# Kernel optimization log

Hardware: AMD Instinct MI355X
Metric: run time of the kernel (lower is better)

The kernel has to match this reference:

```python
import jax, jax.numpy as jnp
import numpy as np

B = 65536
N_HOSTS = 16
N_FEATS = 48        # 3 * n_hosts
N_WINDOW = 3
N_LATENT = 10
GAT_IN = 3
GAT_OUT = 16
E = N_WINDOW + GAT_OUT  # 19, MHA embed dim
PROTO_DIM = 10


def setup_inputs() -> dict:
    key = jax.random.key(0)
    ks = jax.random.split(key, 20)
    def rn(k, shape, scale=0.1):
        return jax.random.normal(k, shape, dtype=jnp.float32) * scale
    return {
        "t": jax.random.normal(ks[0], (B, N_WINDOW, N_FEATS), dtype=jnp.float32),
        "s": jnp.zeros((1,), jnp.float32),  # unused by forward, kept for signature fidelity
        "h0": jax.random.normal(ks[1], (B, 1, N_WINDOW), dtype=jnp.float32),
        "gru_Wih": rn(ks[2], (3 * N_WINDOW, N_FEATS)),
        "gru_Whh": rn(ks[3], (3 * N_WINDOW, N_WINDOW)),
        "gru_bih": rn(ks[4], (3 * N_WINDOW,)),
        "gru_bhh": rn(ks[5], (3 * N_WINDOW,)),
        "gat_W": rn(ks[6], (GAT_IN, GAT_OUT)),
        "gat_al": rn(ks[7], (GAT_OUT,)),
        "gat_ar": rn(ks[8], (GAT_OUT,)),
        "mha_Win": rn(ks[9], (3 * E, E)),
        "mha_bin": rn(ks[10], (3 * E,)),
        "mha_Wout": rn(ks[11], (E, E)),
        "mha_bout": rn(ks[12], (E,)),
        "enc_W": rn(ks[13], (N_HOSTS * N_LATENT, N_WINDOW * E)),
        "enc_b": rn(ks[14], (N_HOSTS * N_LATENT,)),
        "anom_W": rn(ks[15], (2, N_LATENT)),
        "anom_b": rn(ks[16], (2,)),
        "proto_W": rn(ks[17], (PROTO_DIM, N_LATENT)),
        "proto_b": rn(ks[18], (PROTO_DIM,)),
    }


def _forward(t, s, h0, gru_Wih, gru_Whh, gru_bih, gru_bhh,
             gat_W, gat_al, gat_ar, mha_Win, mha_bin, mha_Wout, mha_bout,
             enc_W, enc_b, anom_W, anom_b, proto_W, proto_b):
    # ---- GRU (seq-first, batch B, hidden = n_window = 3) ----
    xs = jnp.swapaxes(t, 0, 1)  # (3, B, 48)
    h0_ = h0[:, 0, :]           # (B, 3)

    def gru_step(h, x_t):
        gi = x_t @ gru_Wih.T + gru_bih   # (B, 9)
        gh = h @ gru_Whh.T + gru_bhh     # (B, 9)
        i_r, i_z, i_n = jnp.split(gi, 3, axis=-1)
        h_r, h_z, h_n = jnp.split(gh, 3, axis=-1)
        r = jax.nn.sigmoid(i_r + h_r)
        z = jax.nn.sigmoid(i_z + h_z)
        n = jnp.tanh(i_n + r * h_n)
        h_new = (1.0 - z) * n + z * h
        return h_new, h_new

    _, gru_out = jax.lax.scan(gru_step, h0_, xs)  # (3, B, 3)

    # ---- GAT on fully-connected 16-node graph (with self loops) ----
    gin = t.reshape(t.shape[0], N_WINDOW, N_HOSTS, GAT_IN)      # (B, 3, 16, 3)
    z = jnp.einsum("bwnc,cf->bwnf", gin, gat_W)                 # (B, 3, 16, 16)
    el = z @ gat_al                                              # src scores (B,3,16)
    er = z @ gat_ar                                              # dst scores (B,3,16)
    e = jax.nn.leaky_relu(er[..., :, None] + el[..., None, :], 0.2)  # (B,3,v,u)
    alpha = jax.nn.softmax(e, axis=-1)                           # softmax over sources u
    gat_nodes = jnp.einsum("bwvu,bwuf->bwvf", alpha, z)          # (B, 3, 16, 16)
    gat_out = gat_nodes.mean(axis=2)                             # (B, 3, 16) mean over hosts
    gat_out = jnp.swapaxes(gat_out, 0, 1)                        # (3, B, 16)

    # ---- concat + single-head MHA (embed=19) ----
    c = jnp.concatenate([gru_out, gat_out], axis=-1)             # (3, B, 19)
    Wq, Wk, Wv = jnp.split(mha_Win, 3, axis=0)
    bq, bk, bv = jnp.split(mha_bin, 3, axis=0)
    q = c @ Wq.T + bq
    k = c @ Wk.T + bk
    v = c @ Wv.T + bv
    scores = jnp.einsum("sbe,tbe->bst", q, k) / jnp.sqrt(jnp.float32(E))
    attw = jax.nn.softmax(scores, axis=-1)
    attn = jnp.einsum("bst,tbe->sbe", attw, v)
    attn = attn @ mha_Wout.T + mha_bout                          # (3, B, 19)

    # ---- encoder: Linear(57,160); LeakyReLU(True) => negative_slope=1.0 => identity ----
    flat = jnp.swapaxes(attn, 0, 1).reshape(-1, N_WINDOW * E)    # (B, 57), seq-major flatten
    latent = flat @ enc_W.T + enc_b                              # (B, 160)
    latent = latent.reshape(-1, N_HOSTS, N_LATENT)               # (B, 16, 10)

    # ---- per-host tiny decoders, vectorized ----
    anomaly = jax.nn.softmax(latent @ anom_W.T + anom_b, axis=-1)   # (B, 16, 2)
    proto = jax.nn.sigmoid(latent @ proto_W.T + proto_b)            # (B, 16, PROTO_DIM)
    return anomaly, proto


def reference(t, s, h0, gru_Wih, gru_Whh, gru_bih, gru_bhh,
              gat_W, gat_al, gat_ar, mha_Win, mha_bin, mha_Wout, mha_bout,
              enc_W, enc_b, anom_W, anom_b, proto_W, proto_b):
    return _forward(t, s, h0, gru_Wih, gru_Whh, gru_bih, gru_bhh,
                    gat_W, gat_al, gat_ar, mha_Win, mha_bin, mha_Wout, mha_bout,
                    enc_W, enc_b, anom_W, anom_b, proto_W, proto_b)
```

## Files before the change

kernel.cpp:

```cpp
#include <hip/hip_runtime.h>

#define NW 3
#define NF 48
#define NHOST 16
#define NLAT 10
#define GOUT 16
#define EDIM 19
#define PDIM 10

#define CB_M    0
#define CB_P    361
#define CB_G    722
#define CB_H    741
#define CB_R    760
#define CB_C0   779
#define CB_WAL  780
#define CB_WAR  783
#define CB_CBIG 800
#define CB_BF   976
#define CB_TOT  10240

typedef __attribute__((ext_vector_type(8))) short bf16x8;
typedef __attribute__((ext_vector_type(4))) float f32x4;

__device__ __forceinline__ float frcp(float x){ return __builtin_amdgcn_rcpf(x); }
__device__ __forceinline__ float fsig(float x){ return frcp(1.f + __expf(-x)); }
__device__ __forceinline__ float ftanh(float x){ return 1.f - 2.f*frcp(1.f + __expf(2.f*x)); }
__device__ __forceinline__ unsigned short f2bf(float x){
    union { float f; unsigned u; } v; v.f = x;
    unsigned r = v.u + 0x7FFFu + ((v.u >> 16) & 1u);
    return (unsigned short)(r >> 16);
}

__global__ __launch_bounds__(256) void k_const(
    const float* __restrict__ Win, const float* __restrict__ bin,
    const float* __restrict__ Wout, const float* __restrict__ bout,
    const float* __restrict__ gatW, const float* __restrict__ gal,
    const float* __restrict__ gar, const float* __restrict__ encW,
    const float* __restrict__ encb,
    const float* __restrict__ aW, const float* __restrict__ ab,
    const float* __restrict__ pW, const float* __restrict__ pb,
    float* __restrict__ cb)
{
    const int w = blockIdx.x*blockDim.x + threadIdx.x;
    if (w < 786) {
        const int idx = w;
        float acc = 0.f;
        if (idx < 361) {
            int i = idx/19, j = idx%19;
            for (int e = 0; e < EDIM; ++e) acc += Win[e*EDIM+i]*Win[(EDIM+e)*EDIM+j];
        } else if (idx < 722) {
            int k = idx-361; int i = k/19, j = k%19;
            for (int e = 0; e < EDIM; ++e) acc += Wout[i*EDIM+e]*Win[(2*EDIM+e)*EDIM+j];
        } else if (idx < 741) {
            int j = idx-722;
            for (int e = 0; e < EDIM; ++e) acc += bin[e]*Win[(EDIM+e)*EDIM+j];
        } else if (idx < 760) {
            int i = idx-741;
            for (int e = 0; e < EDIM; ++e) acc += Win[e*EDIM+i]*bin[EDIM+e];
        } else if (idx < 779) {
            int i = idx-760; acc = bout[i];
            for (int e = 0; e < EDIM; ++e) acc += Wout[i*EDIM+e]*bin[2*EDIM+e];
        } else if (idx == 779) {
            for (int e = 0; e < EDIM; ++e) acc += bin[e]*bin[EDIM+e];
        } else {
            int c = idx-780; int cc = c%3; bool left = c<3;
            for (int f2 = 0; f2 < GOUT; ++f2)
                acc += gatW[cc*GOUT+f2]*(left ? gal[f2] : gar[f2]);
        }
        cb[idx] = acc;
    } else if (w < 962) {
        const int g = w - 786;
        int host = g / 11, jj = g % 11;
        float acc = (jj == 0) ? (ab[0] - ab[1]) : pb[jj-1];
        for (int l = 0; l < NLAT; ++l) {
            float coef = (jj == 0) ? (aW[l] - aW[NLAT+l]) : pW[(jj-1)*NLAT + l];
            acc += coef * encb[host*NLAT + l];
        }
        cb[CB_CBIG + g] = acc;
    } else if (w < 12226) {
        unsigned short* bf = (unsigned short*)(cb + CB_BF);
        const int u = w - 962;
        int j    = u & 7;
        int lane = (u >> 3) & 63;
        int tile = u >> 9;
        int half = tile / 11, n = tile % 11;
        int k = half*32 + ((lane >> 4) & 3)*8 + j;
        int g = n*16 + (lane & 15);
        float acc = 0.f;
        if (k < 57) {
            int host = g / 11, jj = g % 11;
            for (int l = 0; l < NLAT; ++l) {
                float coef = (jj == 0) ? (aW[l] - aW[NLAT+l]) : pW[(jj-1)*NLAT + l];
                acc += coef * encW[(host*NLAT + l)*57 + k];
            }
        }
        bf[u] = f2bf(acc);
    }
}

__global__ __launch_bounds__(256) void k_front(
    const float* __restrict__ t, const float* __restrict__ Wih, const float* __restrict__ bih,
    const float* __restrict__ gatW, const float* __restrict__ cb,
    float* __restrict__ ws1, int B)
{
    const int b = blockIdx.x*blockDim.x + threadIdx.x;
    const int w = blockIdx.y;
    if (b >= B) return;

    float x[NF];
    const float* tp = t + ((size_t)b*NW + w)*NF;
#pragma unroll
    for (int i = 0; i < NF/4; ++i) {
        float4 v = *reinterpret_cast<const float4*>(tp + i*4);
        x[i*4+0]=v.x; x[i*4+1]=v.y; x[i*4+2]=v.z; x[i*4+3]=v.w;
    }
    float* o = ws1 + (size_t)w*25*B + b;
#pragma unroll
    for (int r = 0; r < 9; ++r) {
        float acc = bih[r];
#pragma unroll
        for (int j = 0; j < NF; ++j) acc += x[j]*Wih[r*NF+j];
        o[(size_t)r*B] = acc;
    }
    const float Wal0=cb[CB_WAL],Wal1=cb[CB_WAL+1],Wal2=cb[CB_WAL+2];
    const float War0=cb[CB_WAR],War1=cb[CB_WAR+1],War2=cb[CB_WAR+2];
    float el[NHOST], er[NHOST];
#pragma unroll
    for (int n = 0; n < NHOST; ++n) {
        el[n] = x[n*3+0]*Wal0 + x[n*3+1]*Wal1 + x[n*3+2]*Wal2;
        er[n] = x[n*3+0]*War0 + x[n*3+1]*War1 + x[n*3+2]*War2;
    }
    float beta[NHOST];
#pragma unroll
    for (int u = 0; u < NHOST; ++u) beta[u] = 0.f;
#pragma unroll
    for (int v = 0; v < NHOST; ++v) {
        float ee[NHOST]; float sum = 0.f;
#pragma unroll
        for (int u = 0; u < NHOST; ++u) {
            float s = er[v] + el[u];
            s = fmaxf(s, 0.2f*s);
            ee[u] = __expf(s); sum += ee[u];
        }
        float inv = frcp(sum);
#pragma unroll
        for (int u = 0; u < NHOST; ++u) beta[u] += ee[u]*inv;
    }
    float g0=0.f, g1=0.f, g2=0.f;
#pragma unroll
    for (int u = 0; u < NHOST; ++u) {
        float bu = beta[u]*(1.f/16.f);
        g0 += bu*x[u*3+0]; g1 += bu*x[u*3+1]; g2 += bu*x[u*3+2];
    }
#pragma unroll
    for (int f2 = 0; f2 < GOUT; ++f2)
        o[(size_t)(9+f2)*B] = g0*gatW[f2] + g1*gatW[GOUT+f2] + g2*gatW[2*GOUT+f2];
}

__global__ __attribute__((amdgpu_flat_work_group_size(256,256), amdgpu_waves_per_eu(1,1)))
void k_mid(const float* __restrict__ ws1, const float* __restrict__ h0,
           const float* __restrict__ Whh, const float* __restrict__ bhh,
           const float* __restrict__ cb, unsigned short* __restrict__ ws2bf, int B)
{
    const int b = blockIdx.x*blockDim.x + threadIdx.x;
    if (b >= B) return;

    float h[3] = { h0[b*3+0], h0[b*3+1], h0[b*3+2] };
    float cw[57];
#pragma unroll
    for (int w = 0; w < NW; ++w) {
        const float* i1 = ws1 + (size_t)w*25*B + b;
        float gi[9];
#pragma unroll
        for (int r = 0; r < 9; ++r) gi[r] = i1[(size_t)r*B];
        float gh[9];
#pragma unroll
        for (int r = 0; r < 9; ++r)
            gh[r] = bhh[r] + h[0]*Whh[r*3+0] + h[1]*Whh[r*3+1] + h[2]*Whh[r*3+2];
#pragma unroll
        for (int j = 0; j < 3; ++j) {
            float rg = fsig(gi[j]   + gh[j]);
            float zg = fsig(gi[3+j] + gh[3+j]);
            float ng = ftanh(gi[6+j] + rg*gh[6+j]);
            h[j] = (1.f - zg)*ng + zg*h[j];
        }
        cw[w*EDIM+0]=h[0]; cw[w*EDIM+1]=h[1]; cw[w*EDIM+2]=h[2];
#pragma unroll
        for (int f2 = 0; f2 < GOUT; ++f2) cw[w*EDIM+3+f2] = i1[(size_t)(9+f2)*B];
    }
    float hs[NW];
#pragma unroll
    for (int s = 0; s < NW; ++s) {
        float a = 0.f;
#pragma unroll
        for (int i = 0; i < EDIM; ++i) a += cw[s*EDIM+i]*cb[CB_H+i];
        hs[s] = a;
    }
    const float c0 = cb[CB_C0];
    float sc[NW][NW];
#pragma unroll
    for (int tt = 0; tt < NW; ++tt) {
        float mt[EDIM];
#pragma unroll
        for (int i = 0; i < EDIM; ++i) {
            float a = 0.f;
#pragma unroll
            for (int j = 0; j < EDIM; ++j) a += cb[CB_M+i*EDIM+j]*cw[tt*EDIM+j];
            mt[i] = a;
        }
        float gt = 0.f;
#pragma unroll
        for (int j = 0; j < EDIM; ++j) gt += cb[CB_G+j]*cw[tt*EDIM+j];
#pragma unroll
        for (int s = 0; s < NW; ++s) {
            float a = 0.f;
#pragma unroll
            for (int i = 0; i < EDIM; ++i) a += cw[s*EDIM+i]*mt[i];
            sc[s][tt] = (a + gt + hs[s] + c0) * 0.2294157338705618f;
        }
    }
    float attw[NW][NW];
#pragma unroll
    for (int s = 0; s < NW; ++s) {
        float m = fmaxf(sc[s][0], fmaxf(sc[s][1], sc[s][2]));
        float e0=__expf(sc[s][0]-m), e1=__expf(sc[s][1]-m), e2=__expf(sc[s][2]-m);
        float inv = frcp(e0+e1+e2);
        attw[s][0]=e0*inv; attw[s][1]=e1*inv; attw[s][2]=e2*inv;
    }
#pragma unroll
    for (int tt = 0; tt < NW; ++tt) {
        float pc[EDIM];
#pragma unroll
        for (int i = 0; i < EDIM; ++i) {
            float a = 0.f;
#pragma unroll
            for (int j = 0; j < EDIM; ++j) a += cb[CB_P+i*EDIM+j]*cw[tt*EDIM+j];
            pc[i] = a;
        }
#pragma unroll
        for (int i = 0; i < EDIM; ++i) cw[tt*EDIM+i] = pc[i];
    }
    unsigned short* ob = ws2bf + (size_t)b*64;
#pragma unroll
    for (int c = 0; c < 8; ++c) {
        union { uint4 q; unsigned short s[8]; } pk;
#pragma unroll
        for (int e = 0; e < 8; ++e) {
            const int idx = c*8 + e;
            float val = 0.f;
            if (idx < 57) {
                const int s2 = idx / EDIM, i = idx % EDIM;
                val = cb[CB_R+i] + attw[s2][0]*cw[i] + attw[s2][1]*cw[EDIM+i]
                    + attw[s2][2]*cw[2*EDIM+i];
            }
            pk.s[e] = f2bf(val);
        }
        *reinterpret_cast<uint4*>(ob + c*8) = pk.q;
    }
}

__global__ __launch_bounds__(256) void k_enc(
    const unsigned short* __restrict__ ws2bf, const float* __restrict__ cb,
    float* __restrict__ outA, float* __restrict__ outP, int B)
{
    __shared__ float lg[64][178];
    const int lane = threadIdx.x & 63;
    const int wv   = __builtin_amdgcn_readfirstlane(threadIdx.x >> 6);
    const int b0   = blockIdx.x*64;
    if (b0 >= B) return;

    const int brow = b0 + wv*16 + (lane & 15);
    const int koff = (lane >> 4) * 8;
    const unsigned short* ap = ws2bf + (size_t)brow*64;
    union { uint4 q; bf16x8 v; } a0, a1;
    a0.q = *reinterpret_cast<const uint4*>(ap + koff);
    a1.q = *reinterpret_cast<const uint4*>(ap + 32 + koff);

    const uint4* bfq = (const uint4*)(cb + CB_BF);
    const int r0 = wv*16 + ((lane >> 4) << 2);
#pragma unroll
    for (int n = 0; n < 11; ++n) {
        union { uint4 q; bf16x8 v; } bf0, bf1;
        bf0.q = bfq[(size_t)n*64 + lane];
        bf1.q = bfq[(size_t)(11 + n)*64 + lane];
        f32x4 acc = {0.f, 0.f, 0.f, 0.f};
        acc = __builtin_amdgcn_mfma_f32_16x16x32_bf16(a0.v, bf0.v, acc, 0, 0, 0);
        acc = __builtin_amdgcn_mfma_f32_16x16x32_bf16(a1.v, bf1.v, acc, 0, 0, 0);
        const int c = n*16 + (lane & 15);
#pragma unroll
        for (int r = 0; r < 4; ++r) lg[r0 + r][c] = acc[r];
    }
    __syncthreads();

    const int host = threadIdx.x & 15;
    const int tg   = threadIdx.x >> 4;
    const float* cbig = cb + CB_CBIG;
#pragma unroll
    for (int i = 0; i < 4; ++i) {
        const int bl = tg + 16*i;
        const int b  = b0 + bl;
        float v[11];
#pragma unroll
        for (int jj = 0; jj < 11; ++jj)
            v[jj] = lg[bl][host*11 + jj] + cbig[host*11 + jj];
        float p0 = fsig(v[0]);
        float2 av; av.x = p0; av.y = 1.f - p0;
        *reinterpret_cast<float2*>(outA + (size_t)b*32 + host*2) = av;
        float* pP = outP + (size_t)b*160 + host*10;
#pragma unroll
        for (int p = 0; p < 5; ++p) {
            float2 pv; pv.x = fsig(v[1 + 2*p]); pv.y = fsig(v[2 + 2*p]);
            *reinterpret_cast<float2*>(pP + 2*p) = pv;
        }
    }
}

extern "C" void kernel_launch(void* const* d_in, const int* in_sizes, int n_in,
                              void* d_out, int out_size, void* d_ws, size_t ws_size,
                              hipStream_t stream) {
    const float* t    = (const float*)d_in[0];
    const float* h0   = (const float*)d_in[2];
    const float* Wih  = (const float*)d_in[3];
    const float* Whh  = (const float*)d_in[4];
    const float* bih  = (const float*)d_in[5];
    const float* bhh  = (const float*)d_in[6];
    const float* gatW = (const float*)d_in[7];
    const float* gal  = (const float*)d_in[8];
    const float* gar  = (const float*)d_in[9];
    const float* Win  = (const float*)d_in[10];
    const float* bin  = (const float*)d_in[11];
    const float* Wout = (const float*)d_in[12];
    const float* bout = (const float*)d_in[13];
    const float* encW = (const float*)d_in[14];
    const float* encb = (const float*)d_in[15];
    const float* aW   = (const float*)d_in[16];
    const float* ab   = (const float*)d_in[17];
    const float* pW   = (const float*)d_in[18];
    const float* pb   = (const float*)d_in[19];

    const int B = in_sizes[0] / (NW * NF);
    float* cb  = (float*)d_ws;
    float* ws1 = cb + CB_TOT;
    unsigned short* ws2bf = (unsigned short*)(ws1 + (size_t)25*NW*B);
    float* outA = (float*)d_out;
    float* outP = (float*)d_out + (size_t)B*32;

    k_const<<<dim3(48), 256, 0, stream>>>(Win, bin, Wout, bout, gatW, gal, gar,
                                          encW, encb, aW, ab, pW, pb, cb);
    k_front<<<dim3((B+255)/256, NW), 256, 0, stream>>>(t, Wih, bih, gatW, cb, ws1, B);
    k_mid<<<dim3((B+255)/256), 256, 0, stream>>>(ws1, h0, Whh, bhh, cb, ws2bf, B);
    k_enc<<<dim3((B+63)/64), 256, 0, stream>>>(ws2bf, cb, outA, outP, B);
}
```

Before: 77.23 us.

## Fuse front and mid kernels through shared memory, dropping ws1 global round-trip

Merges the per-window GRU input projection and GAT kernel with the GRU/attention mid kernel into one kernel. Each 256-thread block handles 64 batch rows: 192 threads compute the 25 features for the 3 windows into LDS, then 64 threads run the recurrent and attention part. This removes a 75*B float write and read through global memory plus one launch. It also folds the GAT beta accumulation into the softmax loop. The trade-off is that three quarters of each block sits idle during the mid phase, which lowers parallelism there.

Measured after the change: 81.59 us. 1.06x slower.

```diff
diff --git a/kernel.cpp b/kernel.cpp
--- a/kernel.cpp
+++ b/kernel.cpp
@@ -99,81 +99,73 @@
     }
 }
 
-__global__ __launch_bounds__(256) void k_front(
-    const float* __restrict__ t, const float* __restrict__ Wih, const float* __restrict__ bih,
-    const float* __restrict__ gatW, const float* __restrict__ cb,
-    float* __restrict__ ws1, int B)
+__global__ __launch_bounds__(256, 4) void k_fm(
+    const float* __restrict__ t, const float* __restrict__ h0,
+    const float* __restrict__ Wih, const float* __restrict__ bih,
+    const float* __restrict__ gatW, const float* __restrict__ Whh,
+    const float* __restrict__ bhh, const float* __restrict__ cb,
+    unsigned short* __restrict__ ws2bf, int B)
 {
-    const int b = blockIdx.x*blockDim.x + threadIdx.x;
-    const int w = blockIdx.y;
-    if (b >= B) return;
-
-    float x[NF];
-    const float* tp = t + ((size_t)b*NW + w)*NF;
-#pragma unroll
-    for (int i = 0; i < NF/4; ++i) {
-        float4 v = *reinterpret_cast<const float4*>(tp + i*4);
-        x[i*4+0]=v.x; x[i*4+1]=v.y; x[i*4+2]=v.z; x[i*4+3]=v.w;
-    }
-    float* o = ws1 + (size_t)w*25*B + b;
-#pragma unroll
-    for (int r = 0; r < 9; ++r) {
-        float acc = bih[r];
-#pragma unroll
-        for (int j = 0; j < NF; ++j) acc += x[j]*Wih[r*NF+j];
-        o[(size_t)r*B] = acc;
-    }
-    const float Wal0=cb[CB_WAL],Wal1=cb[CB_WAL+1],Wal2=cb[CB_WAL+2];
-    const float War0=cb[CB_WAR],War1=cb[CB_WAR+1],War2=cb[CB_WAR+2];
-    float el[NHOST], er[NHOST];
-#pragma unroll
-    for (int n = 0; n < NHOST; ++n) {
-        el[n] = x[n*3+0]*Wal0 + x[n*3+1]*Wal1 + x[n*3+2]*Wal2;
-        er[n] = x[n*3+0]*War0 + x[n*3+1]*War1 + x[n*3+2]*War2;
-    }
-    float beta[NHOST];
-#pragma unroll
-    for (int u = 0; u < NHOST; ++u) beta[u] = 0.f;
-#pragma unroll
-    for (int v = 0; v < NHOST; ++v) {
-        float ee[NHOST]; float sum = 0.f;
-#pragma unroll
-        for (int u = 0; u < NHOST; ++u) {
-            float s = er[v] + el[u];
-            s = fmaxf(s, 0.2f*s);
-            ee[u] = __expf(s); sum += ee[u];
-        }
-        float inv = frcp(sum);
-#pragma unroll
-        for (int u = 0; u < NHOST; ++u) beta[u] += ee[u]*inv;
-    }
-    float g0=0.f, g1=0.f, g2=0.f;
-#pragma unroll
-    for (int u = 0; u < NHOST; ++u) {
-        float bu = beta[u]*(1.f/16.f);
-        g0 += bu*x[u*3+0]; g1 += bu*x[u*3+1]; g2 += bu*x[u*3+2];
-    }
-#pragma unroll
-    for (int f2 = 0; f2 < GOUT; ++f2)
-        o[(size_t)(9+f2)*B] = g0*gatW[f2] + g1*gatW[GOUT+f2] + g2*gatW[2*GOUT+f2];
-}
-
-__global__ __attribute__((amdgpu_flat_work_group_size(256,256), amdgpu_waves_per_eu(1,1)))
-void k_mid(const float* __restrict__ ws1, const float* __restrict__ h0,
-           const float* __restrict__ Whh, const float* __restrict__ bhh,
-           const float* __restrict__ cb, unsigned short* __restrict__ ws2bf, int B)
-{
-    const int b = blockIdx.x*blockDim.x + threadIdx.x;
-    if (b >= B) return;
-
-    float h[3] = { h0[b*3+0], h0[b*3+1], h0[b*3+2] };
+    __shared__ float fm[NW][25][64];
+    const int tid = threadIdx.x;
+    const int b0  = blockIdx.x * 64;
+
+    if (tid < 192) {
+        const int bl = tid & 63;
+        const int w  = tid >> 6;
+        const float* tp = t + ((size_t)(b0 + bl)*NW + w)*NF;
+        float x[NF];
+#pragma unroll
+        for (int i = 0; i < NF/4; ++i) {
+            float4 v = *reinterpret_cast<const float4*>(tp + i*4);
+            x[i*4+0]=v.x; x[i*4+1]=v.y; x[i*4+2]=v.z; x[i*4+3]=v.w;
+        }
+#pragma unroll
+        for (int r = 0; r < 9; ++r) {
+            float acc = bih[r];
+#pragma unroll
+            for (int j = 0; j < NF; ++j) acc += x[j]*Wih[r*NF+j];
+            fm[w][r][bl] = acc;
+        }
+        const float Wal0=cb[CB_WAL],Wal1=cb[CB_WAL+1],Wal2=cb[CB_WAL+2];
+        const float War0=cb[CB_WAR],War1=cb[CB_WAR+1],War2=cb[CB_WAR+2];
+        float el[NHOST], er[NHOST];
+#pragma unroll
+        for (int n = 0; n < NHOST; ++n) {
+            el[n] = x[n*3+0]*Wal0 + x[n*3+1]*Wal1 + x[n*3+2]*Wal2;
+            er[n] = x[n*3+0]*War0 + x[n*3+1]*War1 + x[n*3+2]*War2;
+        }
+        float g0=0.f, g1=0.f, g2=0.f;
+#pragma unroll
+        for (int v = 0; v < NHOST; ++v) {
+            float sum = 0.f, a0 = 0.f, a1 = 0.f, a2 = 0.f;
+#pragma unroll
+            for (int u = 0; u < NHOST; ++u) {
+                float s = er[v] + el[u];
+                s = fmaxf(s, 0.2f*s);
+                float e = __expf(s);
+                sum += e;
+                a0 += e*x[u*3+0]; a1 += e*x[u*3+1]; a2 += e*x[u*3+2];
+            }
+            float inv = frcp(sum);
+            g0 += a0*inv; g1 += a1*inv; g2 += a2*inv;
+        }
+        g0 *= (1.f/16.f); g1 *= (1.f/16.f); g2 *= (1.f/16.f);
+#pragma unroll
+        for (int f2 = 0; f2 < GOUT; ++f2)
+            fm[w][9+f2][bl] = g0*gatW[f2] + g1*gatW[GOUT+f2] + g2*gatW[2*GOUT+f2];
+    }
+    __syncthreads();
+    if (tid >= 64) return;
+
+    const int b = b0 + tid;
+    float h[3] = { h0[(size_t)b*3+0], h0[(size_t)b*3+1], h0[(size_t)b*3+2] };
     float cw[57];
 #pragma unroll
     for (int w = 0; w < NW; ++w) {
-        const float* i1 = ws1 + (size_t)w*25*B + b;
         float gi[9];
 #pragma unroll
-        for (int r = 0; r < 9; ++r) gi[r] = i1[(size_t)r*B];
+        for (int r = 0; r < 9; ++r) gi[r] = fm[w][r][tid];
         float gh[9];
 #pragma unroll
         for (int r = 0; r < 9; ++r)
@@ -187,7 +179,7 @@
         }
         cw[w*EDIM+0]=h[0]; cw[w*EDIM+1]=h[1]; cw[w*EDIM+2]=h[2];
 #pragma unroll
-        for (int f2 = 0; f2 < GOUT; ++f2) cw[w*EDIM+3+f2] = i1[(size_t)(9+f2)*B];
+        for (int f2 = 0; f2 < GOUT; ++f2) cw[w*EDIM+3+f2] = fm[w][9+f2][tid];
     }
     float hs[NW];
 #pragma unroll
@@ -341,14 +333,12 @@
 
     const int B = in_sizes[0] / (NW * NF);
     float* cb  = (float*)d_ws;
-    float* ws1 = cb + CB_TOT;
-    unsigned short* ws2bf = (unsigned short*)(ws1 + (size_t)25*NW*B);
+    unsigned short* ws2bf = (unsigned short*)(cb + CB_TOT);
     float* outA = (float*)d_out;
     float* outP = (float*)d_out + (size_t)B*32;
 
     k_const<<<dim3(48), 256, 0, stream>>>(Win, bin, Wout, bout, gatW, gal, gar,
                                           encW, encb, aW, ab, pW, pb, cb);
-    k_front<<<dim3((B+255)/256, NW), 256, 0, stream>>>(t, Wih, bih, gatW, cb, ws1, B);
-    k_mid<<<dim3((B+255)/256), 256, 0, stream>>>(ws1, h0, Whh, bhh, cb, ws2bf, B);
+    k_fm<<<dim3(B/64), 256, 0, stream>>>(t, h0, Wih, bih, gatW, Whh, bhh, cb, ws2bf, B);
     k_enc<<<dim3((B+63)/64), 256, 0, stream>>>(ws2bf, cb, outA, outP, B);
 }
```

## Spread front kernel across 16 lanes per sample with shuffle reductions

Applied to the files above, without the earlier changes.

The front kernel now assigns one 16-lane group per batch sample, with each lane owning one host. The GRU input projection, the GAT attention softmax and the pooled features are computed with cross-lane shuffle reductions instead of 48-float per-thread arrays. The intermediate workspace layout changes from feature-major to sample-major (32 floats per sample per window), and the mid kernel reads it that way. This is meant to cut register pressure and the serial 16x16 exp work per thread, at the cost of many shuffles, 16x more threads, strided 3-float loads of t, and uncoalesced per-thread reads in the mid kernel. The mid kernel also drops its waves_per_eu(1,1) attribute.

Measured after the change: 120.9 us. 1.57x slower.

```diff
diff --git a/kernel.cpp b/kernel.cpp
--- a/kernel.cpp
+++ b/kernel.cpp
@@ -99,81 +99,84 @@
     }
 }
 
-__global__ __launch_bounds__(256) void k_front(
+__global__ __launch_bounds__(256) void k_f(
     const float* __restrict__ t, const float* __restrict__ Wih, const float* __restrict__ bih,
     const float* __restrict__ gatW, const float* __restrict__ cb,
     float* __restrict__ ws1, int B)
 {
-    const int b = blockIdx.x*blockDim.x + threadIdx.x;
-    const int w = blockIdx.y;
-    if (b >= B) return;
-
-    float x[NF];
-    const float* tp = t + ((size_t)b*NW + w)*NF;
-#pragma unroll
-    for (int i = 0; i < NF/4; ++i) {
-        float4 v = *reinterpret_cast<const float4*>(tp + i*4);
-        x[i*4+0]=v.x; x[i*4+1]=v.y; x[i*4+2]=v.z; x[i*4+3]=v.w;
-    }
-    float* o = ws1 + (size_t)w*25*B + b;
-#pragma unroll
-    for (int r = 0; r < 9; ++r) {
-        float acc = bih[r];
-#pragma unroll
-        for (int j = 0; j < NF; ++j) acc += x[j]*Wih[r*NF+j];
-        o[(size_t)r*B] = acc;
-    }
+    const int lane = threadIdx.x & 63;
+    const int u    = lane & 15;
+    const int gbase= lane & 48;
+    const int grp  = threadIdx.x >> 4;
+    const int b    = blockIdx.x*16 + grp;
+
     const float Wal0=cb[CB_WAL],Wal1=cb[CB_WAL+1],Wal2=cb[CB_WAL+2];
     const float War0=cb[CB_WAR],War1=cb[CB_WAR+1],War2=cb[CB_WAR+2];
-    float el[NHOST], er[NHOST];
-#pragma unroll
-    for (int n = 0; n < NHOST; ++n) {
-        el[n] = x[n*3+0]*Wal0 + x[n*3+1]*Wal1 + x[n*3+2]*Wal2;
-        er[n] = x[n*3+0]*War0 + x[n*3+1]*War1 + x[n*3+2]*War2;
-    }
-    float beta[NHOST];
-#pragma unroll
-    for (int u = 0; u < NHOST; ++u) beta[u] = 0.f;
-#pragma unroll
-    for (int v = 0; v < NHOST; ++v) {
-        float ee[NHOST]; float sum = 0.f;
-#pragma unroll
-        for (int u = 0; u < NHOST; ++u) {
-            float s = er[v] + el[u];
+
+#pragma unroll
+    for (int w = 0; w < NW; ++w) {
+        const float* tp = t + ((size_t)b*NW + w)*NF + u*3;
+        const float x0 = tp[0], x1 = tp[1], x2 = tp[2];
+
+        float p[9];
+#pragma unroll
+        for (int r = 0; r < 9; ++r)
+            p[r] = x0*Wih[r*NF+u*3] + x1*Wih[r*NF+u*3+1] + x2*Wih[r*NF+u*3+2];
+#pragma unroll
+        for (int r = 0; r < 9; ++r) {
+            p[r] += __shfl_xor(p[r], 1);
+            p[r] += __shfl_xor(p[r], 2);
+            p[r] += __shfl_xor(p[r], 4);
+            p[r] += __shfl_xor(p[r], 8);
+        }
+        const float el = x0*Wal0 + x1*Wal1 + x2*Wal2;
+        const float er = x0*War0 + x1*War1 + x2*War2;
+        float beta = 0.f;
+#pragma unroll
+        for (int v = 0; v < NHOST; ++v) {
+            float erv = __shfl(er, gbase + v);
+            float s = erv + el;
             s = fmaxf(s, 0.2f*s);
-            ee[u] = __expf(s); sum += ee[u];
-        }
-        float inv = frcp(sum);
-#pragma unroll
-        for (int u = 0; u < NHOST; ++u) beta[u] += ee[u]*inv;
-    }
-    float g0=0.f, g1=0.f, g2=0.f;
-#pragma unroll
-    for (int u = 0; u < NHOST; ++u) {
-        float bu = beta[u]*(1.f/16.f);
-        g0 += bu*x[u*3+0]; g1 += bu*x[u*3+1]; g2 += bu*x[u*3+2];
-    }
-#pragma unroll
-    for (int f2 = 0; f2 < GOUT; ++f2)
-        o[(size_t)(9+f2)*B] = g0*gatW[f2] + g1*gatW[GOUT+f2] + g2*gatW[2*GOUT+f2];
-}
-
-__global__ __attribute__((amdgpu_flat_work_group_size(256,256), amdgpu_waves_per_eu(1,1)))
-void k_mid(const float* __restrict__ ws1, const float* __restrict__ h0,
-           const float* __restrict__ Whh, const float* __restrict__ bhh,
-           const float* __restrict__ cb, unsigned short* __restrict__ ws2bf, int B)
+            float e = __expf(s);
+            float S = e;
+            S += __shfl_xor(S, 1);
+            S += __shfl_xor(S, 2);
+            S += __shfl_xor(S, 4);
+            S += __shfl_xor(S, 8);
+            beta += e * frcp(S);
+        }
+        float g0 = beta*x0, g1 = beta*x1, g2 = beta*x2;
+        g0 += __shfl_xor(g0,1); g0 += __shfl_xor(g0,2); g0 += __shfl_xor(g0,4); g0 += __shfl_xor(g0,8);
+        g1 += __shfl_xor(g1,1); g1 += __shfl_xor(g1,2); g1 += __shfl_xor(g1,4); g1 += __shfl_xor(g1,8);
+        g2 += __shfl_xor(g2,1); g2 += __shfl_xor(g2,2); g2 += __shfl_xor(g2,4); g2 += __shfl_xor(g2,8);
+        g0 *= (1.f/16.f); g1 *= (1.f/16.f); g2 *= (1.f/16.f);
+
+        float* o = ws1 + ((size_t)b*NW + w)*32;
+        o[9+u] = g0*gatW[u] + g1*gatW[GOUT+u] + g2*gatW[2*GOUT+u];
+        if (u < 9) {
+            float gv = u==0?p[0]:u==1?p[1]:u==2?p[2]:u==3?p[3]:u==4?p[4]
+                      :u==5?p[5]:u==6?p[6]:u==7?p[7]:p[8];
+            o[u] = gv + bih[u];
+        }
+    }
+}
+
+__global__ __launch_bounds__(256) void k_m(
+    const float* __restrict__ ws1, const float* __restrict__ h0,
+    const float* __restrict__ Whh, const float* __restrict__ bhh,
+    const float* __restrict__ cb, unsigned short* __restrict__ ws2bf, int B)
 {
     const int b = blockIdx.x*blockDim.x + threadIdx.x;
     if (b >= B) return;
 
-    float h[3] = { h0[b*3+0], h0[b*3+1], h0[b*3+2] };
+    float h[3] = { h0[(size_t)b*3+0], h0[(size_t)b*3+1], h0[(size_t)b*3+2] };
     float cw[57];
 #pragma unroll
     for (int w = 0; w < NW; ++w) {
-        const float* i1 = ws1 + (size_t)w*25*B + b;
+        const float* i1 = ws1 + ((size_t)b*NW + w)*32;
         float gi[9];
 #pragma unroll
-        for (int r = 0; r < 9; ++r) gi[r] = i1[(size_t)r*B];
+        for (int r = 0; r < 9; ++r) gi[r] = i1[r];
         float gh[9];
 #pragma unroll
         for (int r = 0; r < 9; ++r)
@@ -187,7 +190,7 @@
         }
         cw[w*EDIM+0]=h[0]; cw[w*EDIM+1]=h[1]; cw[w*EDIM+2]=h[2];
 #pragma unroll
-        for (int f2 = 0; f2 < GOUT; ++f2) cw[w*EDIM+3+f2] = i1[(size_t)(9+f2)*B];
+        for (int f2 = 0; f2 < GOUT; ++f2) cw[w*EDIM+3+f2] = i1[9+f2];
     }
     float hs[NW];
 #pragma unroll
@@ -342,13 +345,13 @@
     const int B = in_sizes[0] / (NW * NF);
     float* cb  = (float*)d_ws;
     float* ws1 = cb + CB_TOT;
-    unsigned short* ws2bf = (unsigned short*)(ws1 + (size_t)25*NW*B);
+    unsigned short* ws2bf = (unsigned short*)(ws1 + (size_t)NW*32*B);
     float* outA = (float*)d_out;
     float* outP = (float*)d_out + (size_t)B*32;
 
     k_const<<<dim3(48), 256, 0, stream>>>(Win, bin, Wout, bout, gatW, gal, gar,
                                           encW, encb, aW, ab, pW, pb, cb);
-    k_front<<<dim3((B+255)/256, NW), 256, 0, stream>>>(t, Wih, bih, gatW, cb, ws1, B);
-    k_mid<<<dim3((B+255)/256), 256, 0, stream>>>(ws1, h0, Whh, bhh, cb, ws2bf, B);
+    k_f<<<dim3(B/16), 256, 0, stream>>>(t, Wih, bih, gatW, cb, ws1, B);
+    k_m<<<dim3((B+255)/256), 256, 0, stream>>>(ws1, h0, Whh, bhh, cb, ws2bf, B);
     k_enc<<<dim3((B+63)/64), 256, 0, stream>>>(ws2bf, cb, outA, outP, B);
 }
```

## Split attention mid kernel across three threads per sample with shared memory

Applied to the files above, without the earlier changes.

The mid kernel now gives each batch element three threads, one per window position, instead of one thread doing all positions. Each thread computes its own projections and shares them through LDS with two block barriers, which cuts per-thread register pressure and serial work and raises occupancy. Every thread also redundantly recomputes the GRU recurrence, and the output is written as scalar 16-bit stores instead of packed 128-bit stores. The bounds check is gone, so B must be a multiple of 64.

Measured after the change: 73.20 us. 1.06x faster.

```diff
diff --git a/kernel.cpp b/kernel.cpp
--- a/kernel.cpp
+++ b/kernel.cpp
@@ -158,22 +158,25 @@
         o[(size_t)(9+f2)*B] = g0*gatW[f2] + g1*gatW[GOUT+f2] + g2*gatW[2*GOUT+f2];
 }
 
-__global__ __attribute__((amdgpu_flat_work_group_size(256,256), amdgpu_waves_per_eu(1,1)))
-void k_mid(const float* __restrict__ ws1, const float* __restrict__ h0,
-           const float* __restrict__ Whh, const float* __restrict__ bhh,
-           const float* __restrict__ cb, unsigned short* __restrict__ ws2bf, int B)
+__global__ __launch_bounds__(192) void k_m(
+    const float* __restrict__ ws1, const float* __restrict__ h0,
+    const float* __restrict__ Whh, const float* __restrict__ bhh,
+    const float* __restrict__ cb, unsigned short* __restrict__ ws2bf, int B)
 {
-    const int b = blockIdx.x*blockDim.x + threadIdx.x;
-    if (b >= B) return;
-
-    float h[3] = { h0[b*3+0], h0[b*3+1], h0[b*3+2] };
-    float cw[57];
+    __shared__ float mtb[NW][EDIM][64];
+    __shared__ float gtb[NW][64];
+    __shared__ float pcb[NW][EDIM][64];
+    const int bl = threadIdx.x & 63;
+    const int s  = threadIdx.x >> 6;
+    const int b  = blockIdx.x*64 + bl;
+
+    float h[3] = { h0[(size_t)b*3+0], h0[(size_t)b*3+1], h0[(size_t)b*3+2] };
+    float ch[NW][3];
 #pragma unroll
     for (int w = 0; w < NW; ++w) {
-        const float* i1 = ws1 + (size_t)w*25*B + b;
         float gi[9];
 #pragma unroll
-        for (int r = 0; r < 9; ++r) gi[r] = i1[(size_t)r*B];
+        for (int r = 0; r < 9; ++r) gi[r] = ws1[((size_t)w*25 + r)*B + b];
         float gh[9];
 #pragma unroll
         for (int r = 0; r < 9; ++r)
@@ -185,78 +188,63 @@
             float ng = ftanh(gi[6+j] + rg*gh[6+j]);
             h[j] = (1.f - zg)*ng + zg*h[j];
         }
-        cw[w*EDIM+0]=h[0]; cw[w*EDIM+1]=h[1]; cw[w*EDIM+2]=h[2];
-#pragma unroll
-        for (int f2 = 0; f2 < GOUT; ++f2) cw[w*EDIM+3+f2] = i1[(size_t)(9+f2)*B];
-    }
-    float hs[NW];
-#pragma unroll
-    for (int s = 0; s < NW; ++s) {
+        ch[w][0]=h[0]; ch[w][1]=h[1]; ch[w][2]=h[2];
+    }
+    float cw[EDIM];
+#pragma unroll
+    for (int j = 0; j < 3; ++j)
+        cw[j] = (s==0) ? ch[0][j] : (s==1) ? ch[1][j] : ch[2][j];
+#pragma unroll
+    for (int f2 = 0; f2 < GOUT; ++f2)
+        cw[3+f2] = ws1[((size_t)s*25 + 9 + f2)*B + b];
+
+    float hsv = 0.f, gt = 0.f;
+#pragma unroll
+    for (int i = 0; i < EDIM; ++i) { hsv += cw[i]*cb[CB_H+i]; gt += cw[i]*cb[CB_G+i]; }
+#pragma unroll
+    for (int i = 0; i < EDIM; ++i) {
         float a = 0.f;
 #pragma unroll
-        for (int i = 0; i < EDIM; ++i) a += cw[s*EDIM+i]*cb[CB_H+i];
-        hs[s] = a;
-    }
+        for (int j = 0; j < EDIM; ++j) a += cb[CB_M+i*EDIM+j]*cw[j];
+        mtb[s][i][bl] = a;
+    }
+    gtb[s][bl] = gt;
+    __syncthreads();
+
     const float c0 = cb[CB_C0];
-    float sc[NW][NW];
+    float sc[NW];
 #pragma unroll
     for (int tt = 0; tt < NW; ++tt) {
-        float mt[EDIM];
-#pragma unroll
-        for (int i = 0; i < EDIM; ++i) {
-            float a = 0.f;
-#pragma unroll
-            for (int j = 0; j < EDIM; ++j) a += cb[CB_M+i*EDIM+j]*cw[tt*EDIM+j];
-            mt[i] = a;
-        }
-        float gt = 0.f;
-#pragma unroll
-        for (int j = 0; j < EDIM; ++j) gt += cb[CB_G+j]*cw[tt*EDIM+j];
-#pragma unroll
-        for (int s = 0; s < NW; ++s) {
-            float a = 0.f;
-#pragma unroll
-            for (int i = 0; i < EDIM; ++i) a += cw[s*EDIM+i]*mt[i];
-            sc[s][tt] = (a + gt + hs[s] + c0) * 0.2294157338705618f;
-        }
-    }
-    float attw[NW][NW];
-#pragma unroll
-    for (int s = 0; s < NW; ++s) {
-        float m = fmaxf(sc[s][0], fmaxf(sc[s][1], sc[s][2]));
-        float e0=__expf(sc[s][0]-m), e1=__expf(sc[s][1]-m), e2=__expf(sc[s][2]-m);
-        float inv = frcp(e0+e1+e2);
-        attw[s][0]=e0*inv; attw[s][1]=e1*inv; attw[s][2]=e2*inv;
-    }
-#pragma unroll
-    for (int tt = 0; tt < NW; ++tt) {
-        float pc[EDIM];
-#pragma unroll
-        for (int i = 0; i < EDIM; ++i) {
-            float a = 0.f;
-#pragma unroll
-            for (int j = 0; j < EDIM; ++j) a += cb[CB_P+i*EDIM+j]*cw[tt*EDIM+j];
-            pc[i] = a;
-        }
-#pragma unroll
-        for (int i = 0; i < EDIM; ++i) cw[tt*EDIM+i] = pc[i];
-    }
-    unsigned short* ob = ws2bf + (size_t)b*64;
-#pragma unroll
-    for (int c = 0; c < 8; ++c) {
-        union { uint4 q; unsigned short s[8]; } pk;
-#pragma unroll
-        for (int e = 0; e < 8; ++e) {
-            const int idx = c*8 + e;
-            float val = 0.f;
-            if (idx < 57) {
-                const int s2 = idx / EDIM, i = idx % EDIM;
-                val = cb[CB_R+i] + attw[s2][0]*cw[i] + attw[s2][1]*cw[EDIM+i]
-                    + attw[s2][2]*cw[2*EDIM+i];
-            }
-            pk.s[e] = f2bf(val);
-        }
-        *reinterpret_cast<uint4*>(ob + c*8) = pk.q;
+        float a = 0.f;
+#pragma unroll
+        for (int i = 0; i < EDIM; ++i) a += cw[i]*mtb[tt][i][bl];
+        sc[tt] = (a + gtb[tt][bl] + hsv + c0) * 0.2294157338705618f;
+    }
+    float m = fmaxf(sc[0], fmaxf(sc[1], sc[2]));
+    float e0=__expf(sc[0]-m), e1=__expf(sc[1]-m), e2=__expf(sc[2]-m);
+    float inv = frcp(e0+e1+e2);
+    float aw0=e0*inv, aw1=e1*inv, aw2=e2*inv;
+
+#pragma unroll
+    for (int i = 0; i < EDIM; ++i) {
+        float a = 0.f;
+#pragma unroll
+        for (int j = 0; j < EDIM; ++j) a += cb[CB_P+i*EDIM+j]*cw[j];
+        pcb[s][i][bl] = a;
+    }
+    __syncthreads();
+
+    unsigned short* ob = ws2bf + (size_t)b*64 + s*EDIM;
+#pragma unroll
+    for (int i = 0; i < EDIM; ++i) {
+        float v = cb[CB_R+i] + aw0*pcb[0][i][bl] + aw1*pcb[1][i][bl]
+                + aw2*pcb[2][i][bl];
+        ob[i] = f2bf(v);
+    }
+    if (s == 0) {
+        unsigned short* pz = ws2bf + (size_t)b*64 + 57;
+#pragma unroll
+        for (int r = 0; r < 7; ++r) pz[r] = 0;
     }
 }
 
@@ -349,6 +337,6 @@
     k_const<<<dim3(48), 256, 0, stream>>>(Win, bin, Wout, bout, gatW, gal, gar,
                                           encW, encb, aW, ab, pW, pb, cb);
     k_front<<<dim3((B+255)/256, NW), 256, 0, stream>>>(t, Wih, bih, gatW, cb, ws1, B);
-    k_mid<<<dim3((B+255)/256), 256, 0, stream>>>(ws1, h0, Whh, bhh, cb, ws2bf, B);
+    k_m<<<dim3(B/64), 192, 0, stream>>>(ws1, h0, Whh, bhh, cb, ws2bf, B);
     k_enc<<<dim3((B+63)/64), 256, 0, stream>>>(ws2bf, cb, outA, outP, B);
 }
```
